# Kernel optimization log

Hardware: AMD Instinct MI355X
Metric: run time of the kernel (lower is better)

Reference implementation:

```python
import math
import jax, jax.numpy as jnp
import numpy as np

NUM_HEADS = 4
HEAD_DIM = 384


def reshape_fortran(x, shape):
    # column-major (Fortran) reshape, matching the torch reverse-permute trick
    x = jnp.transpose(x, tuple(reversed(range(x.ndim))))
    x = x.reshape(tuple(reversed(shape)))
    return jnp.transpose(x, tuple(reversed(range(len(shape)))))


def rel_pos_rotate(data):
    # data: [b, n_heads, L=2M-1, S] -> [b, n_heads, S, S]
    data = jnp.transpose(data, (0, 2, 3, 1))  # [b, d0=L, d1=S, d2=H]
    b, d0, d1, d2 = data.shape
    data = jnp.concatenate([data, jnp.zeros((b, d1, d1, d2), data.dtype)], axis=1)
    data = reshape_fortran(data, (b, (d0 + d1) * d1, 1, d2))
    data = data[:, :(d1 + d0 - 1) * d1]
    data = reshape_fortran(data, (b, d0 + d1 - 1, d1, d2))
    n = d0 // 2
    data = jnp.swapaxes(data[:, n:n + d1], 1, 2)  # [b, d1, d1, d2]
    return jnp.transpose(data, (0, 3, 1, 2))      # [b, H, S, S]


def setup_inputs() -> dict:
    key = jax.random.key(0)
    ks = jax.random.split(key, 5)
    B, S, D = 4, 920, 1536
    M = 920
    return {
        "hidden_states": jax.random.normal(ks[0], (B, S, D), jnp.float32),
        "q_w": jax.random.normal(ks[1], (D, NUM_HEADS * HEAD_DIM), jnp.float32) * 0.02,
        "k_w": jax.random.normal(ks[2], (D, NUM_HEADS * HEAD_DIM), jnp.float32) * 0.02,
        "v_w": jax.random.normal(ks[3], (D, NUM_HEADS * HEAD_DIM), jnp.float32) * 0.02,
        "dist_emb": jax.random.normal(ks[4], (2 * M - 1, HEAD_DIM), jnp.float32) * 0.02,
    }


def reference(hidden_states, q_w, k_w, v_w, dist_emb):
    B, S, D = hidden_states.shape

    def heads(x):  # [B,S,H*hd] -> [B,H,S,hd]
        return jnp.transpose(x.reshape(B, S, NUM_HEADS, HEAD_DIM), (0, 2, 1, 3))

    # query is pre-scaled by 1/sqrt(head_dim), matching the torch code
    q = heads((hidden_states @ q_w) / math.sqrt(HEAD_DIM))
    k = heads(hidden_states @ k_w)
    v = heads(hidden_states @ v_w)

    scores = jnp.einsum("bhqd,bhkd->bhqk", q, k)  # [B,H,S,S]
    # relative position scores: [B,H,L,S] then skew-rotated into [B,H,S,S]
    rel = jnp.einsum("ld,bhsd->bhls", dist_emb, q)
    scores = scores + rel_pos_rotate(rel)

    probs = jax.nn.softmax(scores, axis=-1)
    ctx = jnp.einsum("bhqk,bhkd->bhqd", probs, v)  # [B,H,S,hd]
    ctx = jnp.transpose(ctx, (0, 2, 1, 3)).reshape(B, S, NUM_HEADS * HEAD_DIM)
    return ctx
```

## Files before the change

kernel.cpp:

```cpp
#include <hip/hip_runtime.h>
#include <cstdint>
#include <cstddef>

#define SEQ   920
#define DM    1536
#define DH    384
#define NHD   4
#define NB    4
#define NBH   16
#define MTOK  3680
#define NREL  1839

typedef short          bf16x8 __attribute__((ext_vector_type(8)));
typedef float          f32x4  __attribute__((ext_vector_type(4)));
typedef unsigned short u16x4  __attribute__((ext_vector_type(4)));
typedef unsigned short u16x8  __attribute__((ext_vector_type(8)));

__device__ __forceinline__ unsigned short f2bf(float f){
  union{float f; unsigned u;} v; v.f = f;
  unsigned r = v.u + 0x7FFFu + ((v.u >> 16) & 1u);
  return (unsigned short)(r >> 16);
}
__device__ __forceinline__ float bf2f(unsigned short h){
  union{unsigned u; float f;} v; v.u = ((unsigned)h) << 16;
  return v.f;
}
__device__ __forceinline__ f32x4 mfma_bf16(bf16x8 a, bf16x8 b, f32x4 c){
  return __builtin_amdgcn_mfma_f32_16x16x32_bf16(a, b, c, 0, 0, 0);
}
__device__ __forceinline__ void gload_lds16(const void* g, void* l){
  __builtin_amdgcn_global_load_lds((const __attribute__((address_space(1))) void*)g,
                                   (__attribute__((address_space(3))) void*)l, 16, 0, 0);
}

__global__ __launch_bounds__(256) void k_f2bf(const float* __restrict__ src,
                                              unsigned short* __restrict__ dst, int n){
  int i = (blockIdx.x * 256 + threadIdx.x) * 4;
  int stride = gridDim.x * 256 * 4;
  for(; i + 3 < n; i += stride){
    f32x4 v = *(const f32x4*)(src + i);
    u16x4 o; o.x = f2bf(v.x); o.y = f2bf(v.y); o.z = f2bf(v.z); o.w = f2bf(v.w);
    *(u16x4*)(dst + i) = o;
  }
}

__global__ __launch_bounds__(256) void k_wt3(const float* __restrict__ qw,
                                             const float* __restrict__ kw,
                                             const float* __restrict__ vw,
                                             unsigned short* __restrict__ wt){
  __shared__ float t[32][33];
  const float* w = blockIdx.z == 0 ? qw : (blockIdx.z == 1 ? kw : vw);
  int k0 = blockIdx.x * 32, n0 = blockIdx.y * 32;
  int tx = threadIdx.x, ty = threadIdx.y;
  #pragma unroll
  for(int j = 0; j < 4; j++)
    t[ty*4+j][tx] = w[(size_t)(k0 + ty*4 + j) * DM + n0 + tx];
  __syncthreads();
  #pragma unroll
  for(int j = 0; j < 4; j++)
    wt[(size_t)(blockIdx.z*DM + n0 + ty*4 + j) * DM + k0 + tx] = f2bf(t[tx][ty*4+j]);
}

template<class Epi>
__device__ __forceinline__ void gemm192(const unsigned short* __restrict__ A, int lda, int Amax,
                                        const unsigned short* __restrict__ B, int ldb, int Bmax,
                                        int K, int m0, int n0, Epi epi){
  __shared__ unsigned short As[3*192*64];
  __shared__ unsigned short Bs[3*192*64];
  const int tid = threadIdx.x;
  const int w = tid >> 6, l = tid & 63;
  const int lg = l >> 4, lo = l & 15;
  const int wm = w >> 2, wn = w & 3;

  const char* ga[3]; const char* gb[3];
  #pragma unroll
  for(int r = 0; r < 3; r++){
    int row = r*64 + (tid >> 3);
    int gslot = (tid & 7) ^ (row & 7);
    int ar = m0 + row; ar = ar < Amax ? ar : Amax - 1;
    ga[r] = (const char*)A + (size_t)ar*lda*2 + gslot*16;
    int br = n0 + row; br = br < Bmax ? br : Bmax - 1;
    gb[r] = (const char*)B + (size_t)br*ldb*2 + gslot*16;
  }
  const int ldst = tid * 16;

  auto stage_pair = [&](int kt, int slot, int r){
    size_t koff = (size_t)kt * 128;
    gload_lds16(ga[r] + koff, (char*)As + slot*24576 + r*8192 + ldst);
    gload_lds16(gb[r] + koff, (char*)Bs + slot*24576 + r*8192 + ldst);
  };

  f32x4 acc[6][3] = {};
  const int sw = (lo & 7) << 4;
  const int nk = (2*K + 127) >> 7;
  const int tb = 2*K - (nk - 1)*128;
  const bool keep0 = (lg*16) < tb;
  const bool keep1 = (64 + lg*16) < tb;

  #pragma unroll
  for(int r = 0; r < 3; r++) stage_pair(0, 0, r);
  #pragma unroll
  for(int r = 0; r < 3; r++) stage_pair(1, 1, r);
  asm volatile("s_waitcnt vmcnt(6)" ::: "memory");
  __builtin_amdgcn_s_barrier();

  int st = 0;
  for(int t = 0; t < nk; t++){
    const bool last = (t == nk - 1);
    const bool pf = (t + 2 < nk);
    const int s2 = st + 2 >= 3 ? st - 1 : st + 2;
    const char* Ab = (const char*)As + st*24576;
    const char* Bb = (const char*)Bs + st*24576;

    bf16x8 bfr[3][2], afr[2][2];

    #pragma unroll
    for(int fj = 0; fj < 3; fj++){
      int row = wn*48 + fj*16 + lo;
      #pragma unroll
      for(int kk = 0; kk < 2; kk++)
        bfr[fj][kk] = *(const bf16x8*)(Bb + row*128 + ((kk*64 + lg*16) ^ sw));
    }
    #pragma unroll
    for(int fi = 0; fi < 2; fi++){
      int row = wm*96 + fi*16 + lo;
      #pragma unroll
      for(int kk = 0; kk < 2; kk++)
        afr[fi][kk] = *(const bf16x8*)(Ab + row*128 + ((kk*64 + lg*16) ^ sw));
    }
    if(pf) stage_pair(t + 2, s2, 0);
    if(last){
      #pragma unroll
      for(int fi = 0; fi < 2; fi++){
        if(!keep0) afr[fi][0] = bf16x8{};
        if(!keep1) afr[fi][1] = bf16x8{};
      }
    }
    __builtin_amdgcn_s_barrier();
    asm volatile("s_waitcnt lgkmcnt(0)" ::: "memory");
    __builtin_amdgcn_s_setprio(1);
    #pragma unroll
    for(int kk = 0; kk < 2; kk++)
      #pragma unroll
      for(int fi = 0; fi < 2; fi++)
        #pragma unroll
        for(int fj = 0; fj < 3; fj++)
          acc[fi][fj] = mfma_bf16(afr[fi][kk], bfr[fj][kk], acc[fi][fj]);
    __builtin_amdgcn_s_setprio(0);
    __builtin_amdgcn_s_barrier();

    #pragma unroll
    for(int fi = 0; fi < 2; fi++){
      int row = wm*96 + (fi + 2)*16 + lo;
      #pragma unroll
      for(int kk = 0; kk < 2; kk++)
        afr[fi][kk] = *(const bf16x8*)(Ab + row*128 + ((kk*64 + lg*16) ^ sw));
    }
    if(pf) stage_pair(t + 2, s2, 1);
    if(last){
      #pragma unroll
      for(int fi = 0; fi < 2; fi++){
        if(!keep0) afr[fi][0] = bf16x8{};
        if(!keep1) afr[fi][1] = bf16x8{};
      }
    }
    __builtin_amdgcn_s_barrier();
    asm volatile("s_waitcnt lgkmcnt(0)" ::: "memory");
    __builtin_amdgcn_s_setprio(1);
    #pragma unroll
    for(int kk = 0; kk < 2; kk++)
      #pragma unroll
      for(int fi = 0; fi < 2; fi++)
        #pragma unroll
        for(int fj = 0; fj < 3; fj++)
          acc[fi + 2][fj] = mfma_bf16(afr[fi][kk], bfr[fj][kk], acc[fi + 2][fj]);
    __builtin_amdgcn_s_setprio(0);
    __builtin_amdgcn_s_barrier();

    #pragma unroll
    for(int fi = 0; fi < 2; fi++){
      int row = wm*96 + (fi + 4)*16 + lo;
      #pragma unroll
      for(int kk = 0; kk < 2; kk++)
        afr[fi][kk] = *(const bf16x8*)(Ab + row*128 + ((kk*64 + lg*16) ^ sw));
    }
    if(pf){
      stage_pair(t + 2, s2, 2);
      asm volatile("s_waitcnt vmcnt(6)" ::: "memory");
    } else if(t + 1 < nk){
      asm volatile("s_waitcnt vmcnt(0)" ::: "memory");
    }
    if(last){
      #pragma unroll
      for(int fi = 0; fi < 2; fi++){
        if(!keep0) afr[fi][0] = bf16x8{};
        if(!keep1) afr[fi][1] = bf16x8{};
      }
    }
    __builtin_amdgcn_s_barrier();
    asm volatile("s_waitcnt lgkmcnt(0)" ::: "memory");
    __builtin_amdgcn_s_setprio(1);
    #pragma unroll
    for(int kk = 0; kk < 2; kk++)
      #pragma unroll
      for(int fi = 0; fi < 2; fi++)
        #pragma unroll
        for(int fj = 0; fj < 3; fj++)
          acc[fi + 4][fj] = mfma_bf16(afr[fi][kk], bfr[fj][kk], acc[fi + 4][fj]);
    __builtin_amdgcn_s_setprio(0);
    __builtin_amdgcn_s_barrier();

    st = st + 1 >= 3 ? 0 : st + 1;
  }

  #pragma unroll
  for(int fi = 0; fi < 6; fi++)
    #pragma unroll
    for(int fj = 0; fj < 3; fj++){
      int m = m0 + wm*96 + fi*16 + lg*4;
      int n = n0 + wn*48 + fj*16 + lo;
      epi(m, n, acc[fi][fj]);
    }
}

__global__ __launch_bounds__(512) void k_proj(const unsigned short* __restrict__ X,
                                              const unsigned short* __restrict__ Wt,
                                              unsigned short* __restrict__ Qb,
                                              unsigned short* __restrict__ Kb,
                                              unsigned short* __restrict__ Vt){
  int bid = blockIdx.x;
  int wg  = (bid & 7) * 60 + (bid >> 3);
  int m0 = (wg % 20) * 192, n0 = (wg / 20) * 192;
  gemm192(X, DM, MTOK, Wt, DM, 3*DM, DM, m0, n0,
    [=] __device__ (int m, int n, f32x4 v4){
      if(m >= MTOK) return;
      int which = n / DM, r = n % DM, h = r / DH, d = r % DH;
      int b = m / SEQ, s = m % SEQ;
      int bh = b * NHD + h;
      if(which == 2){
        u16x4 o;
        o.x = f2bf(v4.x); o.y = f2bf(v4.y); o.z = f2bf(v4.z); o.w = f2bf(v4.w);
        *(u16x4*)(Vt + ((size_t)bh*DH + d)*SEQ + s) = o;
      } else if(which == 0){
        #pragma unroll
        for(int i = 0; i < 4; i++)
          Qb[((size_t)bh*SEQ + s + i)*DH + d] = f2bf(v4[i] * 0.05103103630798287f);
      } else {
        #pragma unroll
        for(int i = 0; i < 4; i++)
          Kb[((size_t)bh*SEQ + s + i)*DH + d] = f2bf(v4[i]);
      }
    });
}

__global__ __launch_bounds__(512) void k_rel(const unsigned short* __restrict__ Qb,
                                             const unsigned short* __restrict__ E,
                                             unsigned short* __restrict__ relS){
  int m0 = blockIdx.x * 192, n0 = blockIdx.y * 192;
  int s0 = m0 % SEQ;
  int qlo = s0, qhi = s0 + 191;
  if(qhi >= SEQ){ qlo = 0; qhi = SEQ - 1; }
  if(n0 + 191 < 919 - qhi || n0 > 1838 - qlo) return;
  gemm192(Qb, DH, NBH*SEQ, E, DH, NREL, DH, m0, n0,
    [=] __device__ (int m, int n, f32x4 v4){
      #pragma unroll
      for(int i = 0; i < 4; i++){
        int mi = m + i;
        if(mi >= NBH*SEQ) continue;
        int q = mi % SEQ;
        int j = n - 919 + q;
        if(j < 0 || j >= SEQ) continue;
        relS[(size_t)mi*SEQ + j] = f2bf(v4[i]);
      }
    });
}

__global__ __launch_bounds__(512) void k_sgemm(const unsigned short* __restrict__ Qb,
                                               const unsigned short* __restrict__ Kb,
                                               unsigned short* __restrict__ P){
  int id = blockIdx.x;
  int idp = (id & 7) * 50 + (id >> 3);
  int bh = idp / 25, r = idp % 25;
  int m0 = (r % 5) * 192, n0 = (r / 5) * 192;
  const unsigned short* A = Qb + (size_t)bh*SEQ*DH;
  const unsigned short* B = Kb + (size_t)bh*SEQ*DH;
  unsigned short* Pbh = P + (size_t)bh*SEQ*SEQ;
  gemm192(A, DH, SEQ, B, DH, SEQ, DH, m0, n0,
    [=] __device__ (int m, int n, f32x4 v4){
      if(n >= SEQ) return;
      #pragma unroll
      for(int i = 0; i < 4; i++){
        int mi = m + i;
        if(mi >= SEQ) continue;
        size_t off = (size_t)mi*SEQ + n;
        float p = __expf(v4[i] + bf2f(Pbh[off]));
        Pbh[off] = f2bf(p);
      }
    });
}

__global__ __launch_bounds__(256) void k_rowsum(const unsigned short* __restrict__ P,
                                                float* __restrict__ rs){
  int w = threadIdx.x >> 6, l = threadIdx.x & 63;
  #pragma unroll
  for(int r = 0; r < 4; r++){
    int row = blockIdx.x * 16 + w * 4 + r;
    size_t base = (size_t)row * SEQ;
    float s = 0.f;
    for(int c = l; c < 115; c += 64){
      u16x8 v = *(const u16x8*)(P + base + (size_t)c*8);
      #pragma unroll
      for(int j = 0; j < 8; j++) s += bf2f(v[j]);
    }
    s += __shfl_xor(s, 1);  s += __shfl_xor(s, 2);  s += __shfl_xor(s, 4);
    s += __shfl_xor(s, 8);  s += __shfl_xor(s, 16); s += __shfl_xor(s, 32);
    if(l == 0) rs[row] = s;
  }
}

__global__ __launch_bounds__(512) void k_pv(const unsigned short* __restrict__ P,
                                            const unsigned short* __restrict__ Vt,
                                            const float* __restrict__ rs,
                                            float* __restrict__ out){
  int id = blockIdx.x;
  int idp = (id & 7) * 20 + (id >> 3);
  int bh = idp / 10, r = idp % 10;
  int m0 = (r % 5) * 192, n0 = (r / 5) * 192;
  const unsigned short* A = P  + (size_t)bh*SEQ*SEQ;
  const unsigned short* B = Vt + (size_t)bh*DH*SEQ;
  const float* rsb = rs + (size_t)bh*SEQ;
  const int b = bh >> 2, h = bh & 3;
  gemm192(A, SEQ, SEQ, B, SEQ, DH, SEQ, m0, n0,
    [=] __device__ (int m, int n, f32x4 v4){
      #pragma unroll
      for(int i = 0; i < 4; i++){
        int mi = m + i;
        if(mi >= SEQ) continue;
        out[((size_t)(b*SEQ + mi))*DM + h*DH + n] = v4[i] / rsb[mi];
      }
    });
}

extern "C" void kernel_launch(void* const* d_in, const int* in_sizes, int n_in,
                              void* d_out, int out_size, void* d_ws, size_t ws_size,
                              hipStream_t stream){
  const float* X  = (const float*)d_in[0];
  const float* qw = (const float*)d_in[1];
  const float* kw = (const float*)d_in[2];
  const float* vw = (const float*)d_in[3];
  const float* de = (const float*)d_in[4];
  float* out = (float*)d_out;
  char* ws = (char*)d_ws;

  unsigned short* Qb   = (unsigned short*)ws;
  unsigned short* Kb   = (unsigned short*)(ws + 11304960);
  unsigned short* Vt   = (unsigned short*)(ws + 22609920);
  unsigned short* relS = (unsigned short*)(ws + 33914880);
  unsigned short* Eb   = (unsigned short*)(ws + 60999680);
  unsigned short* Xb   = (unsigned short*)(ws + 33914880);
  unsigned short* Wt   = (unsigned short*)(ws + 45219840);
  float*          rsum = (float*)ws;

  k_f2bf<<<dim3(2048), dim3(256), 0, stream>>>(X,  Xb, MTOK*DM);
  k_f2bf<<<dim3(690),  dim3(256), 0, stream>>>(de, Eb, NREL*DH);
  k_wt3<<<dim3(48,48,3), dim3(32,8), 0, stream>>>(qw, kw, vw, Wt);
  k_proj<<<dim3(480), dim3(512), 0, stream>>>(Xb, Wt, Qb, Kb, Vt);
  k_rel<<<dim3(77,10), dim3(512), 0, stream>>>(Qb, Eb, relS);
  k_sgemm<<<dim3(400), dim3(512), 0, stream>>>(Qb, Kb, relS);
  k_rowsum<<<dim3(920), dim3(256), 0, stream>>>(relS, rsum);
  k_pv<<<dim3(160), dim3(512), 0, stream>>>(relS, Vt, rsum, out);
}
```

Before: 219.7 us.

## Add 256x256 GEMM tile, fuse rowsum into score GEMM, merge conversion kernels

Introduces a new 256x256 double-buffered bf16 MFMA GEMM and uses it for the QKV projection and the QK^T score kernel, with XCD-aware block remapping. The row-sum pass is folded into the score epilogue through shuffle reductions and LDS atomics, writing per-column-tile partial sums that the PV kernel adds up. The two fp32-to-bf16 conversion launches are merged into one. The aim is to cut launches, the extra read of P, and per-FLOP operand traffic, at the cost of a 128KB LDS footprint and more wasted padding work, since 920 is not a multiple of 256.

```diff
diff --git a/kernel.cpp b/kernel.cpp
--- a/kernel.cpp
+++ b/kernel.cpp
@@ -33,14 +33,25 @@
                                    (__attribute__((address_space(3))) void*)l, 16, 0, 0);
 }
 
-__global__ __launch_bounds__(256) void k_f2bf(const float* __restrict__ src,
-                                              unsigned short* __restrict__ dst, int n){
-  int i = (blockIdx.x * 256 + threadIdx.x) * 4;
-  int stride = gridDim.x * 256 * 4;
-  for(; i + 3 < n; i += stride){
-    f32x4 v = *(const f32x4*)(src + i);
-    u16x4 o; o.x = f2bf(v.x); o.y = f2bf(v.y); o.z = f2bf(v.z); o.w = f2bf(v.w);
-    *(u16x4*)(dst + i) = o;
+__global__ __launch_bounds__(256) void k_prep(const float* __restrict__ X,
+                                              const float* __restrict__ de,
+                                              unsigned short* __restrict__ Xb,
+                                              unsigned short* __restrict__ Eb){
+  if(blockIdx.x < 2048){
+    int i = (blockIdx.x * 256 + threadIdx.x) * 4;
+    const int n = MTOK*DM, stride = 2048 * 256 * 4;
+    for(; i + 3 < n; i += stride){
+      f32x4 v = *(const f32x4*)(X + i);
+      u16x4 o; o.x = f2bf(v.x); o.y = f2bf(v.y); o.z = f2bf(v.z); o.w = f2bf(v.w);
+      *(u16x4*)(Xb + i) = o;
+    }
+  } else {
+    int i = ((blockIdx.x - 2048) * 256 + threadIdx.x) * 4;
+    if(i + 3 < NREL*DH){
+      f32x4 v = *(const f32x4*)(de + i);
+      u16x4 o; o.x = f2bf(v.x); o.y = f2bf(v.y); o.z = f2bf(v.z); o.w = f2bf(v.w);
+      *(u16x4*)(Eb + i) = o;
+    }
   }
 }
 
@@ -59,6 +70,135 @@
   #pragma unroll
   for(int j = 0; j < 4; j++)
     wt[(size_t)(blockIdx.z*DM + n0 + ty*4 + j) * DM + k0 + tx] = f2bf(t[tx][ty*4+j]);
+}
+
+template<class Epi>
+__device__ __forceinline__ void gemm256(const unsigned short* __restrict__ A, int lda, int Amax,
+                                        const unsigned short* __restrict__ B, int ldb, int Bmax,
+                                        int K, int m0, int n0, Epi epi){
+  __shared__ char lds[131072];
+  char* ldsA = lds;
+  char* ldsB = lds + 65536;
+  const int tid = threadIdx.x;
+  const int w = tid >> 6, l = tid & 63;
+  const int lg = l >> 4, lo = l & 15;
+  const int wm = w >> 2, wn = w & 3;
+
+  const int gcol = ((tid & 7) ^ ((tid >> 3) & 7)) * 16;
+  const char* gA[2][2]; const char* gB[2][2];
+  #pragma unroll
+  for(int u = 0; u < 2; u++)
+    #pragma unroll
+    for(int j = 0; j < 2; j++){
+      int ar = m0 + u*128 + j*64 + (tid >> 3); ar = ar < Amax ? ar : Amax - 1;
+      gA[u][j] = (const char*)A + (size_t)ar*lda*2 + gcol;
+      int br = n0 + u*128 + j*64 + (tid >> 3); br = br < Bmax ? br : Bmax - 1;
+      gB[u][j] = (const char*)B + (size_t)br*ldb*2 + gcol;
+    }
+  auto stageA = [&](int kt, int s, int u){
+    size_t koff = (size_t)kt * 128;
+    #pragma unroll
+    for(int j = 0; j < 2; j++)
+      gload_lds16(gA[u][j] + koff, ldsA + s*32768 + u*16384 + j*8192 + tid*16);
+  };
+  auto stageB = [&](int kt, int s, int u){
+    size_t koff = (size_t)kt * 128;
+    #pragma unroll
+    for(int j = 0; j < 2; j++)
+      gload_lds16(gB[u][j] + koff, ldsB + s*32768 + u*16384 + j*8192 + tid*16);
+  };
+
+  f32x4 acc[2][4][4] = {};
+  const int sw = (lo & 7) << 4;
+  const int nk = K >> 6;
+
+  stageB(0, 0, 0); stageB(0, 0, 1); stageA(0, 0, 0); stageA(0, 0, 1);
+  asm volatile("s_waitcnt vmcnt(2)" ::: "memory");
+  __builtin_amdgcn_s_barrier();
+
+  for(int t = 0; t < nk; t++){
+    const int s = t & 1, sn = s ^ 1;
+    const bool pf = (t + 1 < nk);
+    const char* Ab = ldsA + s*32768;
+    const char* Bb = ldsB + s*32768;
+    bf16x8 b0[4], b1[4], ar[4];
+
+    #pragma unroll
+    for(int fj = 0; fj < 4; fj++)
+      b0[fj] = *(const bf16x8*)(Bb + (wn*64 + fj*16 + lo)*128 + ((lg*16) ^ sw));
+    #pragma unroll
+    for(int fi = 0; fi < 4; fi++)
+      ar[fi] = *(const bf16x8*)(Ab + (wm*64 + fi*16 + lo)*128 + ((lg*16) ^ sw));
+    if(pf) stageB(t + 1, sn, 0);
+    __builtin_amdgcn_s_barrier();
+    asm volatile("s_waitcnt lgkmcnt(0)" ::: "memory");
+    __builtin_amdgcn_s_setprio(1);
+    #pragma unroll
+    for(int fi = 0; fi < 4; fi++)
+      #pragma unroll
+      for(int fj = 0; fj < 4; fj++)
+        acc[0][fi][fj] = mfma_bf16(ar[fi], b0[fj], acc[0][fi][fj]);
+    __builtin_amdgcn_s_setprio(0);
+
+    #pragma unroll
+    for(int fj = 0; fj < 4; fj++)
+      b1[fj] = *(const bf16x8*)(Bb + (wn*64 + fj*16 + lo)*128 + ((64 + lg*16) ^ sw));
+    #pragma unroll
+    for(int fi = 0; fi < 4; fi++)
+      ar[fi] = *(const bf16x8*)(Ab + (wm*64 + fi*16 + lo)*128 + ((64 + lg*16) ^ sw));
+    if(pf){ stageB(t + 1, sn, 1);
+            asm volatile("s_waitcnt vmcnt(4)" ::: "memory"); }
+    else  { asm volatile("s_waitcnt vmcnt(0)" ::: "memory"); }
+    __builtin_amdgcn_s_barrier();
+    asm volatile("s_waitcnt lgkmcnt(0)" ::: "memory");
+    __builtin_amdgcn_s_setprio(1);
+    #pragma unroll
+    for(int fi = 0; fi < 4; fi++)
+      #pragma unroll
+      for(int fj = 0; fj < 4; fj++)
+        acc[0][fi][fj] = mfma_bf16(ar[fi], b1[fj], acc[0][fi][fj]);
+    __builtin_amdgcn_s_setprio(0);
+
+    #pragma unroll
+    for(int fi = 0; fi < 4; fi++)
+      ar[fi] = *(const bf16x8*)(Ab + (128 + wm*64 + fi*16 + lo)*128 + ((lg*16) ^ sw));
+    if(pf) stageA(t + 1, sn, 0);
+    __builtin_amdgcn_s_barrier();
+    asm volatile("s_waitcnt lgkmcnt(0)" ::: "memory");
+    __builtin_amdgcn_s_setprio(1);
+    #pragma unroll
+    for(int fi = 0; fi < 4; fi++)
+      #pragma unroll
+      for(int fj = 0; fj < 4; fj++)
+        acc[1][fi][fj] = mfma_bf16(ar[fi], b0[fj], acc[1][fi][fj]);
+    __builtin_amdgcn_s_setprio(0);
+
+    #pragma unroll
+    for(int fi = 0; fi < 4; fi++)
+      ar[fi] = *(const bf16x8*)(Ab + (128 + wm*64 + fi*16 + lo)*128 + ((64 + lg*16) ^ sw));
+    if(pf){ stageA(t + 1, sn, 1);
+            asm volatile("s_waitcnt vmcnt(2)" ::: "memory"); }
+    __builtin_amdgcn_s_barrier();
+    asm volatile("s_waitcnt lgkmcnt(0)" ::: "memory");
+    __builtin_amdgcn_s_setprio(1);
+    #pragma unroll
+    for(int fi = 0; fi < 4; fi++)
+      #pragma unroll
+      for(int fj = 0; fj < 4; fj++)
+        acc[1][fi][fj] = mfma_bf16(ar[fi], b1[fj], acc[1][fi][fj]);
+    __builtin_amdgcn_s_setprio(0);
+  }
+
+  #pragma unroll
+  for(int lh = 0; lh < 2; lh++)
+    #pragma unroll
+    for(int fi = 0; fi < 4; fi++)
+      #pragma unroll
+      for(int fj = 0; fj < 4; fj++){
+        int m = m0 + lh*128 + wm*64 + fi*16 + lg*4;
+        int n = n0 + wn*64 + fj*16 + lo;
+        epi(m, n, acc[lh][fi][fj]);
+      }
 }
 
 template<class Epi>
@@ -223,15 +363,16 @@
     }
 }
 
-__global__ __launch_bounds__(512) void k_proj(const unsigned short* __restrict__ X,
-                                              const unsigned short* __restrict__ Wt,
-                                              unsigned short* __restrict__ Qb,
-                                              unsigned short* __restrict__ Kb,
-                                              unsigned short* __restrict__ Vt){
+__global__ __launch_bounds__(512, 2) void k_proj(const unsigned short* __restrict__ X,
+                                                 const unsigned short* __restrict__ Wt,
+                                                 unsigned short* __restrict__ Qb,
+                                                 unsigned short* __restrict__ Kb,
+                                                 unsigned short* __restrict__ Vt){
   int bid = blockIdx.x;
-  int wg  = (bid & 7) * 60 + (bid >> 3);
-  int m0 = (wg % 20) * 192, n0 = (wg / 20) * 192;
-  gemm192(X, DM, MTOK, Wt, DM, 3*DM, DM, m0, n0,
+  int xcd = bid & 7, idx = bid >> 3;
+  int wg = (xcd < 6 ? xcd*34 : 6*34 + (xcd - 6)*33) + idx;
+  int m0 = (wg % 15) * 256, n0 = (wg / 15) * 256;
+  gemm256(X, DM, MTOK, Wt, DM, 3*DM, DM, m0, n0,
     [=] __device__ (int m, int n, f32x4 v4){
       if(m >= MTOK) return;
       int which = n / DM, r = n % DM, h = r / DH, d = r % DH;
@@ -275,60 +416,59 @@
     });
 }
 
-__global__ __launch_bounds__(512) void k_sgemm(const unsigned short* __restrict__ Qb,
-                                               const unsigned short* __restrict__ Kb,
-                                               unsigned short* __restrict__ P){
-  int id = blockIdx.x;
-  int idp = (id & 7) * 50 + (id >> 3);
-  int bh = idp / 25, r = idp % 25;
-  int m0 = (r % 5) * 192, n0 = (r / 5) * 192;
+__global__ __launch_bounds__(512, 2) void k_sgemm(const unsigned short* __restrict__ Qb,
+                                                  const unsigned short* __restrict__ Kb,
+                                                  unsigned short* __restrict__ P,
+                                                  float* __restrict__ rs2){
+  __shared__ float rsLds[256];
+  if(threadIdx.x < 256) rsLds[threadIdx.x] = 0.f;
+  int bid = blockIdx.x;
+  int wg = (bid & 7) * 32 + (bid >> 3);
+  int bh = wg >> 4, r = wg & 15;
+  int m0 = (r & 3) * 256, n0 = (r >> 2) * 256;
   const unsigned short* A = Qb + (size_t)bh*SEQ*DH;
   const unsigned short* B = Kb + (size_t)bh*SEQ*DH;
   unsigned short* Pbh = P + (size_t)bh*SEQ*SEQ;
-  gemm192(A, DH, SEQ, B, DH, SEQ, DH, m0, n0,
+  const int lo = threadIdx.x & 15;
+  gemm256(A, DH, SEQ, B, DH, SEQ, DH, m0, n0,
     [=] __device__ (int m, int n, f32x4 v4){
-      if(n >= SEQ) return;
+      float s[4];
       #pragma unroll
       for(int i = 0; i < 4; i++){
         int mi = m + i;
-        if(mi >= SEQ) continue;
-        size_t off = (size_t)mi*SEQ + n;
-        float p = __expf(v4[i] + bf2f(Pbh[off]));
-        Pbh[off] = f2bf(p);
+        float p = 0.f;
+        if(mi < SEQ && n < SEQ){
+          size_t off = (size_t)mi*SEQ + n;
+          p = __expf(v4[i] + bf2f(Pbh[off]));
+          Pbh[off] = f2bf(p);
+        }
+        s[i] = p;
+      }
+      #pragma unroll
+      for(int i = 0; i < 4; i++){
+        float v = s[i];
+        v += __shfl_xor(v, 1); v += __shfl_xor(v, 2);
+        v += __shfl_xor(v, 4); v += __shfl_xor(v, 8);
+        if(lo == 0) atomicAdd(&rsLds[m - m0 + i], v);
       }
     });
-}
-
-__global__ __launch_bounds__(256) void k_rowsum(const unsigned short* __restrict__ P,
-                                                float* __restrict__ rs){
-  int w = threadIdx.x >> 6, l = threadIdx.x & 63;
-  #pragma unroll
-  for(int r = 0; r < 4; r++){
-    int row = blockIdx.x * 16 + w * 4 + r;
-    size_t base = (size_t)row * SEQ;
-    float s = 0.f;
-    for(int c = l; c < 115; c += 64){
-      u16x8 v = *(const u16x8*)(P + base + (size_t)c*8);
-      #pragma unroll
-      for(int j = 0; j < 8; j++) s += bf2f(v[j]);
-    }
-    s += __shfl_xor(s, 1);  s += __shfl_xor(s, 2);  s += __shfl_xor(s, 4);
-    s += __shfl_xor(s, 8);  s += __shfl_xor(s, 16); s += __shfl_xor(s, 32);
-    if(l == 0) rs[row] = s;
+  __syncthreads();
+  if(threadIdx.x < 256){
+    int row = m0 + threadIdx.x;
+    if(row < SEQ) rs2[(((size_t)(n0 >> 8))*NBH + bh)*SEQ + row] = rsLds[threadIdx.x];
   }
 }
 
 __global__ __launch_bounds__(512) void k_pv(const unsigned short* __restrict__ P,
                                             const unsigned short* __restrict__ Vt,
-                                            const float* __restrict__ rs,
+                                            const float* __restrict__ rs2,
                                             float* __restrict__ out){
-  int id = blockIdx.x;
-  int idp = (id & 7) * 20 + (id >> 3);
+  int bid = blockIdx.x;
+  int idp = (bid & 7) * 20 + (bid >> 3);
   int bh = idp / 10, r = idp % 10;
   int m0 = (r % 5) * 192, n0 = (r / 5) * 192;
   const unsigned short* A = P  + (size_t)bh*SEQ*SEQ;
   const unsigned short* B = Vt + (size_t)bh*DH*SEQ;
-  const float* rsb = rs + (size_t)bh*SEQ;
   const int b = bh >> 2, h = bh & 3;
   gemm192(A, SEQ, SEQ, B, SEQ, DH, SEQ, m0, n0,
     [=] __device__ (int m, int n, f32x4 v4){
@@ -336,7 +476,11 @@
       for(int i = 0; i < 4; i++){
         int mi = m + i;
         if(mi >= SEQ) continue;
-        out[((size_t)(b*SEQ + mi))*DM + h*DH + n] = v4[i] / rsb[mi];
+        float den = rs2[(size_t)bh*SEQ + mi]
+                  + rs2[((size_t)1*NBH + bh)*SEQ + mi]
+                  + rs2[((size_t)2*NBH + bh)*SEQ + mi]
+                  + rs2[((size_t)3*NBH + bh)*SEQ + mi];
+        out[((size_t)(b*SEQ + mi))*DM + h*DH + n] = v4[i] / den;
       }
     });
 }
@@ -359,14 +503,12 @@
   unsigned short* Eb   = (unsigned short*)(ws + 60999680);
   unsigned short* Xb   = (unsigned short*)(ws + 33914880);
   unsigned short* Wt   = (unsigned short*)(ws + 45219840);
-  float*          rsum = (float*)ws;
-
-  k_f2bf<<<dim3(2048), dim3(256), 0, stream>>>(X,  Xb, MTOK*DM);
-  k_f2bf<<<dim3(690),  dim3(256), 0, stream>>>(de, Eb, NREL*DH);
+  float*          rs2  = (float*)(ws + 60999680);
+
+  k_prep<<<dim3(2738), dim3(256), 0, stream>>>(X, de, Xb, Eb);
   k_wt3<<<dim3(48,48,3), dim3(32,8), 0, stream>>>(qw, kw, vw, Wt);
-  k_proj<<<dim3(480), dim3(512), 0, stream>>>(Xb, Wt, Qb, Kb, Vt);
+  k_proj<<<dim3(270), dim3(512), 0, stream>>>(Xb, Wt, Qb, Kb, Vt);
   k_rel<<<dim3(77,10), dim3(512), 0, stream>>>(Qb, Eb, relS);
-  k_sgemm<<<dim3(400), dim3(512), 0, stream>>>(Qb, Kb, relS);
-  k_rowsum<<<dim3(920), dim3(256), 0, stream>>>(relS, rsum);
-  k_pv<<<dim3(160), dim3(512), 0, stream>>>(relS, Vt, rsum, out);
-}
+  k_sgemm<<<dim3(256), dim3(512), 0, stream>>>(Qb, Kb, relS, rs2);
+  k_pv<<<dim3(160), dim3(512), 0, stream>>>(relS, Vt, rs2, out);
+}
```

New measurement: 236.8 us. +7.8%, slower.
